# Optimization experiments

Measured on AMD Instinct MI355X. Metric: run time of the kernel, lower is better.

## Reference

```python
import jax, jax.numpy as jnp
import numpy as np

EPS = 1e-8
NMS_K = 15          # soft_nms_3d window
COM_NMS = 7.0       # soft_nms_3d com_strength
COM_SCORE = 100.0   # score_com_strength
COM_SCALE = 100.0   # scale_com_strength


def conv2d(x, w, b=None, pad=1, groups=1):
    y = jax.lax.conv_general_dilated(
        x, w, (1, 1), [(pad, pad), (pad, pad)],
        dimension_numbers=('NCHW', 'OIHW', 'NCHW'),
        feature_group_count=groups)
    if b is not None:
        y = y + b[None, :, None, None]
    return y


def bn(x, s, b):  # folded inference batchnorm: scale + shift per channel
    return x * s[None, :, None, None] + b[None, :, None, None]


def maxpool_same(x, k):
    p = k // 2
    return jax.lax.reduce_window(x, -jnp.inf, jax.lax.max,
                                 (1, 1, k, k), (1, 1, 1, 1),
                                 [(0, 0), (0, 0), (p, p), (p, p)])


def boxsum_same(x, k):
    p = k // 2
    return jax.lax.reduce_window(x, 0.0, jax.lax.add,
                                 (1, 1, k, k), (1, 1, 1, 1),
                                 [(0, 0), (0, 0), (p, p), (p, p)])


def instance_norm(x, eps=1e-5):  # no affine (nn.InstanceNorm2d default)
    mu = x.mean(axis=(2, 3), keepdims=True)
    var = x.var(axis=(2, 3), keepdims=True)
    return (x - mu) * jax.lax.rsqrt(var + eps)


def inverted_residual(x, dw_w, bna_s, bna_b, pw_w, bnb_s, bnb_b):
    # expand_ratio=1, stride=1, inp==oup -> residual connection
    h = conv2d(x, dw_w, pad=1, groups=x.shape[1])
    h = jnp.clip(bn(h, bna_s, bna_b), 0.0, 6.0)       # ReLU6
    h = conv2d(h, pw_w, pad=0)
    h = bn(h, bnb_s, bnb_b)
    return x + h


def forward(photos, w0, b0, dw1_w, bn1a_s, bn1a_b, pw1_w, bn1b_s, bn1b_b,
            dw2_w, bn2a_s, bn2a_b, pw2_w, bn2b_s, bn2b_b, ws, bs, scale_list):
    x = conv2d(photos, w0, b0)                                   # (B,16,H,W)
    x = inverted_residual(x, dw1_w, bn1a_s, bn1a_b, pw1_w, bn1b_s, bn1b_b)
    x = inverted_residual(x, dw2_w, bn2a_s, bn2a_b, pw2_w, bn2b_s, bn2b_b)
    s = conv2d(x, ws, bs)                                        # (B,C,H,W) C=scales
    s = jax.nn.leaky_relu(instance_norm(s), negative_slope=0.01)

    # ---- soft_nms_3d: windowed competitive softmax over (scale, 15x15) ----
    m = maxpool_same(s, NMS_K).max(axis=1, keepdims=True)        # (B,1,H,W)
    e = jnp.exp(COM_NMS * (s - m))                               # (B,C,H,W)
    sum_e = boxsum_same(e.sum(axis=1, keepdims=True), NMS_K)     # (B,1,H,W)
    probs = e / (sum_e + EPS)                                    # (B,C,H,W)

    # ---- soft_max_and_argmax_1d over scale dim ----
    mx = probs.max(axis=1, keepdims=True)
    e1 = jnp.exp(COM_SCORE * (probs - mx))
    p1 = e1 / (e1.sum(axis=1, keepdims=True) + EPS)
    e2 = jnp.exp(COM_SCALE * (probs - mx))
    p2 = e2 / (e2.sum(axis=1, keepdims=True) + EPS)
    score_map = (probs * p1).sum(axis=1, keepdims=True)          # (B,1,H,W)
    scale_map = (scale_list[None, :, None, None] * p2).sum(axis=1, keepdims=True)
    # return channel-last like the torch code (B,H,W,1)
    return (score_map.transpose(0, 2, 3, 1), scale_map.transpose(0, 2, 3, 1))


def setup_inputs() -> dict:
    key = jax.random.key(0)
    ks = jax.random.split(key, 20)
    B, H, W, C, S = 4, 512, 512, 16, 10
    rn = lambda k, sh, sc=0.1: (jax.random.normal(k, sh, jnp.float32) * sc)
    inp = {
        'photos': jax.random.normal(ks[0], (B, 1, H, W), jnp.float32),
        'w0': rn(ks[1], (C, 1, 3, 3)), 'b0': rn(ks[2], (C,)),
        'dw1_w': rn(ks[3], (C, 1, 3, 3)),
        'bn1a_s': jax.random.uniform(ks[4], (C,), jnp.float32, 0.5, 1.5),
        'bn1a_b': rn(ks[5], (C,)),
        'pw1_w': rn(ks[6], (C, C, 1, 1)),
        'bn1b_s': jax.random.uniform(ks[7], (C,), jnp.float32, 0.5, 1.5),
        'bn1b_b': rn(ks[8], (C,)),
        'dw2_w': rn(ks[9], (C, 1, 3, 3)),
        'bn2a_s': jax.random.uniform(ks[10], (C,), jnp.float32, 0.5, 1.5),
        'bn2a_b': rn(ks[11], (C,)),
        'pw2_w': rn(ks[12], (C, C, 1, 1)),
        'bn2b_s': jax.random.uniform(ks[13], (C,), jnp.float32, 0.5, 1.5),
        'bn2b_b': rn(ks[14], (C,)),
        'ws': rn(ks[15], (S, C, 3, 3)), 'bs': rn(ks[16], (S,)),
        'scale_list': jnp.linspace(3.0, 21.0, S, dtype=jnp.float32),
    }
    return inp


def reference(photos, w0, b0, dw1_w, bn1a_s, bn1a_b, pw1_w, bn1b_s, bn1b_b,
              dw2_w, bn2a_s, bn2a_b, pw2_w, bn2b_s, bn2b_b, ws, bs, scale_list):
    return forward(photos, w0, b0, dw1_w, bn1a_s, bn1a_b, pw1_w, bn1b_s, bn1b_b,
                   dw2_w, bn2a_s, bn2a_b, pw2_w, bn2b_s, bn2b_b, ws, bs, scale_list)
```

## Files before the change

### kernel.cpp

```cpp
#include <hip/hip_runtime.h>
#include <hip/hip_bf16.h>

#define Bn 4
#define Hn 512
#define Wn 512
#define Cn 16
#define Sn 10
#define HWn (Hn*Wn)
#define BHW (Bn*HWn)
#define NG (BHW/4)

__device__ __forceinline__ void load_row6(const float* __restrict__ rp, bool valid,
                                          int w0, float* r) {
    if (valid) {
        float4 v = *reinterpret_cast<const float4*>(rp + w0);
        r[1] = v.x; r[2] = v.y; r[3] = v.z; r[4] = v.w;
        r[0] = (w0 > 0)   ? rp[w0 - 1] : 0.f;
        r[5] = (w0 < 508) ? rp[w0 + 4] : 0.f;
    } else {
        r[0] = r[1] = r[2] = r[3] = r[4] = r[5] = 0.f;
    }
}

__global__ __launch_bounds__(256) void k_conv0(const float* __restrict__ photos,
        const float* __restrict__ w0v, const float* __restrict__ b0,
        float* __restrict__ out) {
    __shared__ float wp[Cn*12];
    __shared__ float sb[Cn];
    int t = threadIdx.x;
    if (t < Cn*9) { int o = t / 9, k = t % 9; wp[o*12 + k] = w0v[t]; }
    if (t < Cn) sb[t] = b0[t];
    __syncthreads();
    int idx = blockIdx.x * 256 + t;
    int w0 = (idx & 127) << 2, h = (idx >> 7) & 511, b = idx >> 16;
    const float* pb = photos + (b << 18);
    float xr[3][6];
    #pragma unroll
    for (int dy = 0; dy < 3; ++dy) {
        int hh = h + dy - 1;
        load_row6(pb + (hh << 9), (unsigned)hh < 512u, w0, xr[dy]);
    }
    #pragma unroll
    for (int o = 0; o < Cn; ++o) {
        float4 wa = *(const float4*)&wp[o*12];
        float4 wb = *(const float4*)&wp[o*12 + 4];
        float wk8 = wp[o*12 + 8];
        float wk[9] = {wa.x, wa.y, wa.z, wa.w, wb.x, wb.y, wb.z, wb.w, wk8};
        float bv = sb[o];
        float a0 = bv, a1 = bv, a2 = bv, a3 = bv;
        #pragma unroll
        for (int dy = 0; dy < 3; ++dy)
            #pragma unroll
            for (int dx = 0; dx < 3; ++dx) {
                float wv = wk[dy*3 + dx];
                a0 += xr[dy][dx + 0] * wv;
                a1 += xr[dy][dx + 1] * wv;
                a2 += xr[dy][dx + 2] * wv;
                a3 += xr[dy][dx + 3] * wv;
            }
        float4 r; r.x = a0; r.y = a1; r.z = a2; r.w = a3;
        *reinterpret_cast<float4*>(out + ((b*Cn + o) << 18) + (h << 9) + w0) = r;
    }
}


struct StageRegs { float4 b0, b1; float hl, hr; };

__device__ __forceinline__ StageRegs stage_load(const float* __restrict__ xc,
                                                int w0, int h0, int t) {
    StageRegs r;
    {
        int row = t >> 5, c4 = t & 31;
        int gh = h0 - 1 + row;
        r.b0 = make_float4(0.f, 0.f, 0.f, 0.f);
        if ((unsigned)gh < 512u)
            r.b0 = *reinterpret_cast<const float4*>(xc + (gh << 9) + w0 + (c4 << 2));
    }
    r.b1 = make_float4(0.f, 0.f, 0.f, 0.f);
    if (t < 64) {
        int s = t + 256;
        int row = s >> 5, c4 = s & 31;
        int gh = h0 - 1 + row;
        if ((unsigned)gh < 512u)
            r.b1 = *reinterpret_cast<const float4*>(xc + (gh << 9) + w0 + (c4 << 2));
    }
    r.hl = 0.f; r.hr = 0.f;
    if (t < 10) {
        int gh = h0 - 1 + t;
        if (w0 > 0 && (unsigned)gh < 512u) r.hl = xc[(gh << 9) + w0 - 1];
    }
    if (t >= 32 && t < 42) {
        int gh = h0 - 1 + (t - 32);
        if (w0 + 128 < 512 && (unsigned)gh < 512u) r.hr = xc[(gh << 9) + w0 + 128];
    }
    return r;
}

__device__ __forceinline__ void stage_write(float (*tile)[128], float* hL, float* hR,
                                            const StageRegs& r, int t) {
    *reinterpret_cast<float4*>(&tile[t >> 5][(t & 31) << 2]) = r.b0;
    if (t < 64) {
        int s = t + 256;
        *reinterpret_cast<float4*>(&tile[s >> 5][(s & 31) << 2]) = r.b1;
    }
    if (t < 10) hL[t] = r.hl;
    if (t >= 32 && t < 42) hR[t - 32] = r.hr;
}

#define READ_ROWS(tilebuf, hLbuf, hRbuf)                                        \
    float4 v_[3]; float lft_[3], rgt_[3];                                       \
    _Pragma("unroll")                                                           \
    for (int dy = 0; dy < 3; ++dy) {                                            \
        v_[dy] = *reinterpret_cast<const float4*>(&(tilebuf)[th + dy][tw << 2]);\
        float l_ = __shfl_up(v_[dy].w, 1);                                      \
        if (tw == 0) l_ = (hLbuf)[th + dy];                                     \
        float rr_ = __shfl_down(v_[dy].x, 1);                                   \
        if (tw == 31) rr_ = (hRbuf)[th + dy];                                   \
        lft_[dy] = l_; rgt_[dy] = rr_;                                          \
    }

__global__ __launch_bounds__(256) void k_ir(const float* __restrict__ x,
        float* __restrict__ y, const float* __restrict__ dww,
        const float* __restrict__ as_, const float* __restrict__ ab_,
        const float* __restrict__ pww, const float* __restrict__ bs_,
        const float* __restrict__ bb_) {
    __shared__ float tile[2][10][128];
    __shared__ float hLs[2][10], hRs[2][10];
    __shared__ float dwp[Cn*12];
    __shared__ float pwT[Cn*Cn];
    __shared__ float sas[Cn], sab[Cn], sbs[Cn], sbb[Cn];
    int t = threadIdx.x;
    { int o = t >> 4, i = t & 15; pwT[i*16 + o] = pww[t]; }
    if (t < Cn*9)  { int c = t / 9, k = t % 9; dwp[c*12 + k] = dww[t]; }
    if (t < Cn) { sas[t] = as_[t]; sab[t] = ab_[t]; }
    if (t >= 64 && t < 64 + Cn) { sbs[t-64] = bs_[t-64]; sbb[t-64] = bb_[t-64]; }

    int bx = blockIdx.x;
    int wt = bx & 3, ht = (bx >> 2) & 63, b = bx >> 8;
    int w0 = wt << 7, h0 = ht << 3;
    int tw = t & 31, th = t >> 5;
    const float* xb = x + ((size_t)b << 22);

    float acc[Cn][4];
    #pragma unroll
    for (int o = 0; o < Cn; ++o) { acc[o][0] = acc[o][1] = acc[o][2] = acc[o][3] = 0.f; }

    StageRegs sr = stage_load(xb, w0, h0, t);
    stage_write(tile[0], hLs[0], hRs[0], sr, t);
    __syncthreads();

    #pragma unroll 1
    for (int c = 0; c < Cn; ++c) {
        if (c + 1 < Cn) sr = stage_load(xb + ((c + 1) << 18), w0, h0, t);
        int bf = c & 1;
        READ_ROWS(tile[bf], hLs[bf], hRs[bf]);
        float4 wa = *(const float4*)&dwp[c*12];
        float4 wb = *(const float4*)&dwp[c*12 + 4];
        float wk8 = dwp[c*12 + 8];
        float wk[9] = {wa.x, wa.y, wa.z, wa.w, wb.x, wb.y, wb.z, wb.w, wk8};
        float t0 = 0.f, t1 = 0.f, t2 = 0.f, t3 = 0.f;
        #pragma unroll
        for (int dy = 0; dy < 3; ++dy) {
            float r6[6] = {lft_[dy], v_[dy].x, v_[dy].y, v_[dy].z, v_[dy].w, rgt_[dy]};
            #pragma unroll
            for (int dx = 0; dx < 3; ++dx) {
                float wv = wk[dy*3 + dx];
                t0 += r6[dx + 0] * wv;
                t1 += r6[dx + 1] * wv;
                t2 += r6[dx + 2] * wv;
                t3 += r6[dx + 3] * wv;
            }
        }
        float sc = sas[c], sh = sab[c];
        t0 = fminf(fmaxf(t0*sc + sh, 0.f), 6.f);
        t1 = fminf(fmaxf(t1*sc + sh, 0.f), 6.f);
        t2 = fminf(fmaxf(t2*sc + sh, 0.f), 6.f);
        t3 = fminf(fmaxf(t3*sc + sh, 0.f), 6.f);
        #pragma unroll
        for (int o4 = 0; o4 < 4; ++o4) {
            float4 wq = *(const float4*)&pwT[c*16 + o4*4];
            acc[o4*4+0][0] += t0*wq.x; acc[o4*4+0][1] += t1*wq.x;
            acc[o4*4+0][2] += t2*wq.x; acc[o4*4+0][3] += t3*wq.x;
            acc[o4*4+1][0] += t0*wq.y; acc[o4*4+1][1] += t1*wq.y;
            acc[o4*4+1][2] += t2*wq.y; acc[o4*4+1][3] += t3*wq.y;
            acc[o4*4+2][0] += t0*wq.z; acc[o4*4+2][1] += t1*wq.z;
            acc[o4*4+2][2] += t2*wq.z; acc[o4*4+2][3] += t3*wq.z;
            acc[o4*4+3][0] += t0*wq.w; acc[o4*4+3][1] += t1*wq.w;
            acc[o4*4+3][2] += t2*wq.w; acc[o4*4+3][3] += t3*wq.w;
        }
        if (c + 1 < Cn) {
            int nb = (c + 1) & 1;
            stage_write(tile[nb], hLs[nb], hRs[nb], sr, t);
            __syncthreads();
        }
    }
    int h = h0 + th, wg = w0 + (tw << 2);
    #pragma unroll
    for (int o = 0; o < Cn; ++o) {
        const float* xo = xb + (o << 18) + (h << 9) + wg;
        float4 xv = *(const float4*)xo;
        float sc = sbs[o], sh = sbb[o];
        float4 r;
        r.x = xv.x + acc[o][0]*sc + sh;
        r.y = xv.y + acc[o][1]*sc + sh;
        r.z = xv.z + acc[o][2]*sc + sh;
        r.w = xv.w + acc[o][3]*sc + sh;
        *reinterpret_cast<float4*>(y + ((size_t)b << 22) + (o << 18) + (h << 9) + wg) = r;
    }
}

__global__ __launch_bounds__(256) void k_convs(const float* __restrict__ x,
        const float* __restrict__ wsw, const float* __restrict__ bsv,
        float* __restrict__ s) {
    __shared__ float tile[2][10][128];
    __shared__ float hLs[2][10], hRs[2][10];
    __shared__ float wp[Cn*Sn*12];
    __shared__ float sb[Sn];
    int t = threadIdx.x;
    for (int i = t; i < Sn*Cn*9; i += 256) {
        int o = i / (Cn*9), r = i % (Cn*9), c = r / 9, k = r % 9;
        wp[(c*Sn + o)*12 + k] = wsw[i];
    }
    if (t < Sn) sb[t] = bsv[t];

    int bx = blockIdx.x;
    int wt = bx & 3, ht = (bx >> 2) & 63, b = bx >> 8;
    int w0 = wt << 7, h0 = ht << 3;
    int tw = t & 31, th = t >> 5;
    const float* xb = x + ((size_t)b << 22);

    float acc[Sn][4];
    #pragma unroll
    for (int o = 0; o < Sn; ++o) {
        float bv = bsv[o];
        acc[o][0] = bv; acc[o][1] = bv; acc[o][2] = bv; acc[o][3] = bv;
    }

    StageRegs sr = stage_load(xb, w0, h0, t);
    stage_write(tile[0], hLs[0], hRs[0], sr, t);
    __syncthreads();

    #pragma unroll 1
    for (int c = 0; c < Cn; ++c) {
        if (c + 1 < Cn) sr = stage_load(xb + ((c + 1) << 18), w0, h0, t);
        int bf = c & 1;
        READ_ROWS(tile[bf], hLs[bf], hRs[bf]);
        #pragma unroll
        for (int o = 0; o < Sn; ++o) {
            const float* wb_ = &wp[(c*Sn + o)*12];
            float4 wa = *(const float4*)wb_;
            float4 wv2 = *(const float4*)(wb_ + 4);
            float wk8 = wb_[8];
            float wk[9] = {wa.x, wa.y, wa.z, wa.w, wv2.x, wv2.y, wv2.z, wv2.w, wk8};
            #pragma unroll
            for (int dy = 0; dy < 3; ++dy) {
                float r6[6] = {lft_[dy], v_[dy].x, v_[dy].y, v_[dy].z, v_[dy].w, rgt_[dy]};
                #pragma unroll
                for (int dx = 0; dx < 3; ++dx) {
                    float wv = wk[dy*3 + dx];
                    acc[o][0] += r6[dx + 0] * wv;
                    acc[o][1] += r6[dx + 1] * wv;
                    acc[o][2] += r6[dx + 2] * wv;
                    acc[o][3] += r6[dx + 3] * wv;
                }
            }
        }
        if (c + 1 < Cn) {
            int nb = (c + 1) & 1;
            stage_write(tile[nb], hLs[nb], hRs[nb], sr, t);
            __syncthreads();
        }
    }
    int h = h0 + th, wg = w0 + (tw << 2);
    #pragma unroll
    for (int o = 0; o < Sn; ++o) {
        float4 r; r.x = acc[o][0]; r.y = acc[o][1]; r.z = acc[o][2]; r.w = acc[o][3];
        *reinterpret_cast<float4*>(s + ((b*Sn + o) << 18) + (h << 9) + wg) = r;
    }
}

__global__ __launch_bounds__(256) void k_in_part(const float* __restrict__ s,
                                                 double* __restrict__ part) {
    int bc = blockIdx.x >> 5, ch = blockIdx.x & 31;
    const float4* p4 = (const float4*)(s + ((size_t)bc << 18) + (ch << 13));
    int t = threadIdx.x;
    double sum = 0.0, sq = 0.0;
    #pragma unroll
    for (int i = 0; i < 8; ++i) {
        float4 v = p4[t + i * 256];
        sum += (double)v.x + (double)v.y + (double)v.z + (double)v.w;
        sq  += (double)v.x*v.x + (double)v.y*v.y + (double)v.z*v.z + (double)v.w*v.w;
    }
    __shared__ double ssum[256], ssq[256];
    ssum[t] = sum; ssq[t] = sq;
    __syncthreads();
    for (int off = 128; off > 0; off >>= 1) {
        if (t < off) { ssum[t] += ssum[t + off]; ssq[t] += ssq[t + off]; }
        __syncthreads();
    }
    if (t == 0) {
        part[blockIdx.x * 2]     = ssum[0];
        part[blockIdx.x * 2 + 1] = ssq[0];
    }
}

__global__ __launch_bounds__(64) void k_in_fin(const double* __restrict__ part,
                                               float2* __restrict__ stats) {
    int bc = blockIdx.x;
    int t = threadIdx.x;
    double sum = 0.0, sq = 0.0;
    if (t < 32) { sum = part[(bc * 32 + t) * 2]; sq = part[(bc * 32 + t) * 2 + 1]; }
    #pragma unroll
    for (int off = 32; off > 0; off >>= 1) {
        sum += __shfl_xor(sum, off);
        sq  += __shfl_xor(sq, off);
    }
    if (t == 0) {
        double mu = sum / (double)HWn;
        double var = sq / (double)HWn - mu * mu;
        float2 st; st.x = (float)mu; st.y = rsqrtf((float)var + 1e-5f);
        stats[bc] = st;
    }
}

__device__ __forceinline__ float nrm(float v, float2 st) {
    float r = (v - st.x) * st.y;
    return r >= 0.f ? r : 0.01f * r;
}

__global__ __launch_bounds__(256) void k_chan_rowmax(const float* __restrict__ s,
        const float2* __restrict__ stats, float* __restrict__ m1) {
    __shared__ float rowbuf[512];
    int bh = blockIdx.x;
    int b = bh >> 9, h = bh & 511;
    int t = threadIdx.x, w0 = t << 1;
    const float* sp = s + ((size_t)(b * Sn) << 18) + (h << 9) + w0;
    float mx0 = -INFINITY, mx1 = -INFINITY;
    #pragma unroll
    for (int c = 0; c < Sn; ++c) {
        float2 st = stats[b * Sn + c];
        float2 v = *reinterpret_cast<const float2*>(sp + ((size_t)c << 18));
        mx0 = fmaxf(mx0, nrm(v.x, st));
        mx1 = fmaxf(mx1, nrm(v.y, st));
    }
    rowbuf[w0] = mx0; rowbuf[w0 + 1] = mx1;
    __syncthreads();
    float2 o;
    {
        int lo = max(w0 - 7, 0), hi = min(w0 + 7, 511);
        float m = -INFINITY;
        for (int ww = lo; ww <= hi; ++ww) m = fmaxf(m, rowbuf[ww]);
        o.x = m;
        int w1 = w0 + 1;
        lo = max(w1 - 7, 0); hi = min(w1 + 7, 511);
        m = -INFINITY;
        for (int ww = lo; ww <= hi; ++ww) m = fmaxf(m, rowbuf[ww]);
        o.y = m;
    }
    *reinterpret_cast<float2*>(m1 + (bh << 9) + w0) = o;
}

__global__ __launch_bounds__(256) void k_col_expsum(const float* __restrict__ s,
        const float2* __restrict__ stats, const float* __restrict__ m1,
        float* __restrict__ mfull, float* __restrict__ tout) {
    __shared__ float esbuf[512];
    int bh = blockIdx.x;
    int b = bh >> 9, h = bh & 511;
    int t = threadIdx.x, w0 = t << 1;
    int lo = max(h - 7, 0), hi = min(h + 7, 511);
    float2 m = make_float2(-INFINITY, -INFINITY);
    for (int hh = lo; hh <= hi; ++hh) {
        float2 v = *reinterpret_cast<const float2*>(m1 + ((size_t)b << 18) + (hh << 9) + w0);
// ... 62 lines not shown
    #pragma unroll
    for (int c = 0; c < Sn; ++c) {
        e0[c] = expf(100.f * (pr0[c] - mx0)); s0 += e0[c];
        e1[c] = expf(100.f * (pr1[c] - mx1)); s1 += e1[c];
    }
    float i0 = 1.f / (s0 + 1e-8f), i1 = 1.f / (s1 + 1e-8f);
    float sc0 = 0.f, sc1 = 0.f, sl0 = 0.f, sl1 = 0.f;
    #pragma unroll
    for (int c = 0; c < Sn; ++c) {
        float p0 = e0[c] * i0, p1 = e1[c] * i1;
        sc0 += pr0[c] * p0; sl0 += sscale[c] * p0;
        sc1 += pr1[c] * p1; sl1 += sscale[c] * p1;
    }
    int oi = (bh << 9) + w0;
    float2 r0; r0.x = sc0; r0.y = sc1;
    float2 r1; r1.x = sl0; r1.y = sl1;
    *reinterpret_cast<float2*>(out + oi) = r0;
    *reinterpret_cast<float2*>(out + BHW + oi) = r1;
}

extern "C" void kernel_launch(void* const* d_in, const int* in_sizes, int n_in,
                              void* d_out, int out_size, void* d_ws, size_t ws_size,
                              hipStream_t stream) {
    const float* photos = (const float*)d_in[0];
    const float* w0     = (const float*)d_in[1];
    const float* b0     = (const float*)d_in[2];
    const float* dw1_w  = (const float*)d_in[3];
    const float* bn1a_s = (const float*)d_in[4];
    const float* bn1a_b = (const float*)d_in[5];
    const float* pw1_w  = (const float*)d_in[6];
    const float* bn1b_s = (const float*)d_in[7];
    const float* bn1b_b = (const float*)d_in[8];
    const float* dw2_w  = (const float*)d_in[9];
    const float* bn2a_s = (const float*)d_in[10];
    const float* bn2a_b = (const float*)d_in[11];
    const float* pw2_w  = (const float*)d_in[12];
    const float* bn2b_s = (const float*)d_in[13];
    const float* bn2b_b = (const float*)d_in[14];
    const float* ws_w   = (const float*)d_in[15];
    const float* bs_v   = (const float*)d_in[16];
    const float* scl    = (const float*)d_in[17];

    char* wsb = (char*)d_ws;
    float* A  = (float*)(wsb);
    float* Bb = (float*)(wsb + 67108864);
    float* S  = (float*)(wsb + 134217728);
    float2* stats = (float2*)Bb;
    double* part  = (double*)(Bb + 1024);
    float* M1 = A;
    float* M  = A + 1 * (1 << 20);
    float* T  = A + 2 * (1 << 20);

    dim3 blk(256);
    int gNG   = NG / 256;
    int gTILE = 4 * 64 * Bn;
    int gROW  = Bn * Hn;

    k_conv0<<<gNG, blk, 0, stream>>>(photos, w0, b0, A);
    k_ir<<<gTILE, blk, 0, stream>>>(A, Bb, dw1_w, bn1a_s, bn1a_b, pw1_w, bn1b_s, bn1b_b);
    k_ir<<<gTILE, blk, 0, stream>>>(Bb, A, dw2_w, bn2a_s, bn2a_b, pw2_w, bn2b_s, bn2b_b);
    k_convs<<<gTILE, blk, 0, stream>>>(A, ws_w, bs_v, S);
    k_in_part<<<Bn * Sn * 32, blk, 0, stream>>>(S, part);
    k_in_fin<<<Bn * Sn, dim3(64), 0, stream>>>(part, stats);
    k_chan_rowmax<<<gROW, blk, 0, stream>>>(S, stats, M1);
    k_col_expsum<<<gROW, blk, 0, stream>>>(S, stats, M1, M, T);
    k_final<<<gROW, blk, 0, stream>>>(S, stats, M, T, scl, (float*)d_out);
}
```

Measured before the change: 215.4 us.

## Retile IR and score convs to 4x128 tiles staging four channels per barrier

Changes the k_ir and k_convs tiling from 8x128 output tiles with 4 pixels per thread to 4x128 tiles with 2 pixels per thread, doubling the grid. Each pipeline stage now stages four input channels at once into padded shared rows with halo columns, replacing per-channel syncs and warp shuffles with direct shared-memory neighbour reads. The aim is fewer barriers, lower register pressure and higher occupancy. The cost is a larger vertical halo overhead (6 rows loaded per 4 output rows instead of 10 per 8) and narrower global stores.

```diff
diff --git a/kernel.cpp b/kernel.cpp
--- a/kernel.cpp
+++ b/kernel.cpp
@@ -64,59 +64,65 @@
 }
 
 
-struct StageRegs { float4 b0, b1; float hl, hr; };
-
-__device__ __forceinline__ StageRegs stage_load(const float* __restrict__ xc,
-                                                int w0, int h0, int t) {
-    StageRegs r;
+#define RSTR 132
+
+struct SR { float4 q0, q1, q2; float hl, hr; };
+
+__device__ __forceinline__ float4 body_ld(const float* __restrict__ base,
+                                          int s, int w0, int h0) {
+    int ch = s / 192, rem = s - ch * 192, rr = rem >> 5, q = rem & 31;
+    int gh = h0 - 1 + rr;
+    float4 v = make_float4(0.f, 0.f, 0.f, 0.f);
+    if ((unsigned)gh < 512u)
+        v = *reinterpret_cast<const float4*>(base + (ch << 18) + (gh << 9) + w0 + (q << 2));
+    return v;
+}
+
+__device__ __forceinline__ SR st_load(const float* __restrict__ base,
+                                      int w0, int h0, int t) {
+    SR r;
+    r.q0 = body_ld(base, t,       w0, h0);
+    r.q1 = body_ld(base, t + 256, w0, h0);
+    r.q2 = body_ld(base, t + 512, w0, h0);
+    r.hl = 0.f; r.hr = 0.f;
+    if (t < 24) {
+        int ch = t / 6, rr = t % 6, gh = h0 - 1 + rr;
+        if (w0 > 0 && (unsigned)gh < 512u) r.hl = base[(ch << 18) + (gh << 9) + w0 - 1];
+    }
+    if (t >= 64 && t < 88) {
+        int u = t - 64, ch = u / 6, rr = u % 6, gh = h0 - 1 + rr;
+        if (w0 + 128 < 512 && (unsigned)gh < 512u) r.hr = base[(ch << 18) + (gh << 9) + w0 + 128];
+    }
+    return r;
+}
+
+__device__ __forceinline__ void st_write(float* __restrict__ buf,
+                                         const SR& r, int t) {
     {
-        int row = t >> 5, c4 = t & 31;
-        int gh = h0 - 1 + row;
-        r.b0 = make_float4(0.f, 0.f, 0.f, 0.f);
-        if ((unsigned)gh < 512u)
-            r.b0 = *reinterpret_cast<const float4*>(xc + (gh << 9) + w0 + (c4 << 2));
-    }
-    r.b1 = make_float4(0.f, 0.f, 0.f, 0.f);
-    if (t < 64) {
-        int s = t + 256;
-        int row = s >> 5, c4 = s & 31;
-        int gh = h0 - 1 + row;
-        if ((unsigned)gh < 512u)
-            r.b1 = *reinterpret_cast<const float4*>(xc + (gh << 9) + w0 + (c4 << 2));
-    }
-    r.hl = 0.f; r.hr = 0.f;
-    if (t < 10) {
-        int gh = h0 - 1 + t;
-        if (w0 > 0 && (unsigned)gh < 512u) r.hl = xc[(gh << 9) + w0 - 1];
-    }
-    if (t >= 32 && t < 42) {
-        int gh = h0 - 1 + (t - 32);
-        if (w0 + 128 < 512 && (unsigned)gh < 512u) r.hr = xc[(gh << 9) + w0 + 128];
-    }
-    return r;
-}
-
-__device__ __forceinline__ void stage_write(float (*tile)[128], float* hL, float* hR,
-                                            const StageRegs& r, int t) {
-    *reinterpret_cast<float4*>(&tile[t >> 5][(t & 31) << 2]) = r.b0;
-    if (t < 64) {
-        int s = t + 256;
-        *reinterpret_cast<float4*>(&tile[s >> 5][(s & 31) << 2]) = r.b1;
-    }
-    if (t < 10) hL[t] = r.hl;
-    if (t >= 32 && t < 42) hR[t - 32] = r.hr;
-}
-
-#define READ_ROWS(tilebuf, hLbuf, hRbuf)                                        \
-    float4 v_[3]; float lft_[3], rgt_[3];                                       \
+        int s = t;       int ch = s / 192, rem = s - ch * 192, rr = rem >> 5, q = rem & 31;
+        *reinterpret_cast<float4*>(buf + (ch * 6 + rr) * RSTR + (q << 2)) = r.q0;
+    }
+    {
+        int s = t + 256; int ch = s / 192, rem = s - ch * 192, rr = rem >> 5, q = rem & 31;
+        *reinterpret_cast<float4*>(buf + (ch * 6 + rr) * RSTR + (q << 2)) = r.q1;
+    }
+    {
+        int s = t + 512; int ch = s / 192, rem = s - ch * 192, rr = rem >> 5, q = rem & 31;
+        *reinterpret_cast<float4*>(buf + (ch * 6 + rr) * RSTR + (q << 2)) = r.q2;
+    }
+    if (t < 24)              buf[((t / 6) * 6 + (t % 6)) * RSTR + 129] = r.hl;
+    if (t >= 64 && t < 88) { int u = t - 64; buf[((u / 6) * 6 + (u % 6)) * RSTR + 128] = r.hr; }
+}
+
+#define LOAD_X(bufp, j)                                                         \
+    float xl_[3], x0_[3], x1_[3], xr_[3];                                       \
     _Pragma("unroll")                                                           \
     for (int dy = 0; dy < 3; ++dy) {                                            \
-        v_[dy] = *reinterpret_cast<const float4*>(&(tilebuf)[th + dy][tw << 2]);\
-        float l_ = __shfl_up(v_[dy].w, 1);                                      \
-        if (tw == 0) l_ = (hLbuf)[th + dy];                                     \
-        float rr_ = __shfl_down(v_[dy].x, 1);                                   \
-        if (tw == 31) rr_ = (hRbuf)[th + dy];                                   \
-        lft_[dy] = l_; rgt_[dy] = rr_;                                          \
+        const float* rp_ = (bufp) + ((j) * 6 + row + dy) * RSTR;                \
+        float2 v_ = *reinterpret_cast<const float2*>(rp_ + 2 * col2);           \
+        x0_[dy] = v_.x; x1_[dy] = v_.y;                                         \
+        xr_[dy] = rp_[2 * col2 + 2];                                            \
+        xl_[dy] = (col2 == 0) ? rp_[129] : rp_[2 * col2 - 1];                   \
     }
 
 __global__ __launch_bounds__(256) void k_ir(const float* __restrict__ x,
@@ -124,8 +130,7 @@
         const float* __restrict__ as_, const float* __restrict__ ab_,
         const float* __restrict__ pww, const float* __restrict__ bs_,
         const float* __restrict__ bb_) {
-    __shared__ float tile[2][10][128];
-    __shared__ float hLs[2][10], hRs[2][10];
+    __shared__ float tile[2][4 * 6 * RSTR];
     __shared__ float dwp[Cn*12];
     __shared__ float pwT[Cn*Cn];
     __shared__ float sas[Cn], sab[Cn], sbs[Cn], sbb[Cn];
@@ -136,146 +141,133 @@
     if (t >= 64 && t < 64 + Cn) { sbs[t-64] = bs_[t-64]; sbb[t-64] = bb_[t-64]; }
 
     int bx = blockIdx.x;
-    int wt = bx & 3, ht = (bx >> 2) & 63, b = bx >> 8;
-    int w0 = wt << 7, h0 = ht << 3;
-    int tw = t & 31, th = t >> 5;
+    int wt = bx & 3, ht = (bx >> 2) & 127, b = bx >> 9;
+    int w0 = wt << 7, h0 = ht << 2;
+    int row = t >> 6, col2 = t & 63;
     const float* xb = x + ((size_t)b << 22);
 
-    float acc[Cn][4];
-    #pragma unroll
-    for (int o = 0; o < Cn; ++o) { acc[o][0] = acc[o][1] = acc[o][2] = acc[o][3] = 0.f; }
-
-    StageRegs sr = stage_load(xb, w0, h0, t);
-    stage_write(tile[0], hLs[0], hRs[0], sr, t);
+    float acc[Cn][2];
+    #pragma unroll
+    for (int o = 0; o < Cn; ++o) { acc[o][0] = 0.f; acc[o][1] = 0.f; }
+
+    SR sr = st_load(xb, w0, h0, t);
+    st_write(tile[0], sr, t);
     __syncthreads();
 
     #pragma unroll 1
-    for (int c = 0; c < Cn; ++c) {
-        if (c + 1 < Cn) sr = stage_load(xb + ((c + 1) << 18), w0, h0, t);
-        int bf = c & 1;
-        READ_ROWS(tile[bf], hLs[bf], hRs[bf]);
-        float4 wa = *(const float4*)&dwp[c*12];
-        float4 wb = *(const float4*)&dwp[c*12 + 4];
-        float wk8 = dwp[c*12 + 8];
-        float wk[9] = {wa.x, wa.y, wa.z, wa.w, wb.x, wb.y, wb.z, wb.w, wk8};
-        float t0 = 0.f, t1 = 0.f, t2 = 0.f, t3 = 0.f;
+    for (int g = 0; g < 4; ++g) {
+        SR nxt;
+        bool more = (g + 1 < 4);
+        if (more) nxt = st_load(xb + ((g + 1) * 4 << 18), w0, h0, t);
+        const float* bufp = tile[g & 1];
         #pragma unroll
-        for (int dy = 0; dy < 3; ++dy) {
-            float r6[6] = {lft_[dy], v_[dy].x, v_[dy].y, v_[dy].z, v_[dy].w, rgt_[dy]};
+        for (int j = 0; j < 4; ++j) {
+            int cc = g * 4 + j;
+            LOAD_X(bufp, j);
+            float4 wa = *(const float4*)&dwp[cc*12];
+            float4 wb = *(const float4*)&dwp[cc*12 + 4];
+            float wk8 = dwp[cc*12 + 8];
+            float wk[9] = {wa.x, wa.y, wa.z, wa.w, wb.x, wb.y, wb.z, wb.w, wk8};
+            float t0 = 0.f, t1 = 0.f;
             #pragma unroll
-            for (int dx = 0; dx < 3; ++dx) {
-                float wv = wk[dy*3 + dx];
-                t0 += r6[dx + 0] * wv;
-                t1 += r6[dx + 1] * wv;
-                t2 += r6[dx + 2] * wv;
-                t3 += r6[dx + 3] * wv;
+            for (int dy = 0; dy < 3; ++dy) {
+                float k0 = wk[dy*3], k1 = wk[dy*3+1], k2 = wk[dy*3+2];
+                t0 += xl_[dy]*k0 + x0_[dy]*k1 + x1_[dy]*k2;
+                t1 += x0_[dy]*k0 + x1_[dy]*k1 + xr_[dy]*k2;
+            }
+            float sc = sas[cc], sh = sab[cc];
+            t0 = fminf(fmaxf(t0*sc + sh, 0.f), 6.f);
+            t1 = fminf(fmaxf(t1*sc + sh, 0.f), 6.f);
+            #pragma unroll
+            for (int o4 = 0; o4 < 4; ++o4) {
+                float4 wq = *(const float4*)&pwT[cc*16 + o4*4];
+                acc[o4*4+0][0] += t0*wq.x; acc[o4*4+0][1] += t1*wq.x;
+                acc[o4*4+1][0] += t0*wq.y; acc[o4*4+1][1] += t1*wq.y;
+                acc[o4*4+2][0] += t0*wq.z; acc[o4*4+2][1] += t1*wq.z;
+                acc[o4*4+3][0] += t0*wq.w; acc[o4*4+3][1] += t1*wq.w;
             }
         }
-        float sc = sas[c], sh = sab[c];
-        t0 = fminf(fmaxf(t0*sc + sh, 0.f), 6.f);
-        t1 = fminf(fmaxf(t1*sc + sh, 0.f), 6.f);
-        t2 = fminf(fmaxf(t2*sc + sh, 0.f), 6.f);
-        t3 = fminf(fmaxf(t3*sc + sh, 0.f), 6.f);
-        #pragma unroll
-        for (int o4 = 0; o4 < 4; ++o4) {
-            float4 wq = *(const float4*)&pwT[c*16 + o4*4];
-            acc[o4*4+0][0] += t0*wq.x; acc[o4*4+0][1] += t1*wq.x;
-            acc[o4*4+0][2] += t2*wq.x; acc[o4*4+0][3] += t3*wq.x;
-            acc[o4*4+1][0] += t0*wq.y; acc[o4*4+1][1] += t1*wq.y;
-            acc[o4*4+1][2] += t2*wq.y; acc[o4*4+1][3] += t3*wq.y;
-            acc[o4*4+2][0] += t0*wq.z; acc[o4*4+2][1] += t1*wq.z;
-            acc[o4*4+2][2] += t2*wq.z; acc[o4*4+2][3] += t3*wq.z;
-            acc[o4*4+3][0] += t0*wq.w; acc[o4*4+3][1] += t1*wq.w;
-            acc[o4*4+3][2] += t2*wq.w; acc[o4*4+3][3] += t3*wq.w;
-        }
-        if (c + 1 < Cn) {
-            int nb = (c + 1) & 1;
-            stage_write(tile[nb], hLs[nb], hRs[nb], sr, t);
+        if (more) {
+            st_write(tile[(g + 1) & 1], nxt, t);
             __syncthreads();
         }
     }
-    int h = h0 + th, wg = w0 + (tw << 2);
+    int h = h0 + row, wg = w0 + (col2 << 1);
     #pragma unroll
     for (int o = 0; o < Cn; ++o) {
-        const float* xo = xb + (o << 18) + (h << 9) + wg;
-        float4 xv = *(const float4*)xo;
+        size_t oi = ((size_t)b << 22) + (o << 18) + (h << 9) + wg;
+        float2 xv = *reinterpret_cast<const float2*>(x + oi);
         float sc = sbs[o], sh = sbb[o];
-        float4 r;
+        float2 r;
         r.x = xv.x + acc[o][0]*sc + sh;
         r.y = xv.y + acc[o][1]*sc + sh;
-        r.z = xv.z + acc[o][2]*sc + sh;
-        r.w = xv.w + acc[o][3]*sc + sh;
-        *reinterpret_cast<float4*>(y + ((size_t)b << 22) + (o << 18) + (h << 9) + wg) = r;
+        *reinterpret_cast<float2*>(y + oi) = r;
     }
 }
 
 __global__ __launch_bounds__(256) void k_convs(const float* __restrict__ x,
         const float* __restrict__ wsw, const float* __restrict__ bsv,
         float* __restrict__ s) {
-    __shared__ float tile[2][10][128];
-    __shared__ float hLs[2][10], hRs[2][10];
+    __shared__ float tile[2][4 * 6 * RSTR];
     __shared__ float wp[Cn*Sn*12];
-    __shared__ float sb[Sn];
     int t = threadIdx.x;
     for (int i = t; i < Sn*Cn*9; i += 256) {
         int o = i / (Cn*9), r = i % (Cn*9), c = r / 9, k = r % 9;
         wp[(c*Sn + o)*12 + k] = wsw[i];
     }
-    if (t < Sn) sb[t] = bsv[t];
 
     int bx = blockIdx.x;
-    int wt = bx & 3, ht = (bx >> 2) & 63, b = bx >> 8;
-    int w0 = wt << 7, h0 = ht << 3;
-    int tw = t & 31, th = t >> 5;
+    int wt = bx & 3, ht = (bx >> 2) & 127, b = bx >> 9;
+    int w0 = wt << 7, h0 = ht << 2;
+    int row = t >> 6, col2 = t & 63;
     const float* xb = x + ((size_t)b << 22);
 
-    float acc[Sn][4];
+    float acc[Sn][2];
     #pragma unroll
     for (int o = 0; o < Sn; ++o) {
         float bv = bsv[o];
-        acc[o][0] = bv; acc[o][1] = bv; acc[o][2] = bv; acc[o][3] = bv;
-    }
-
-    StageRegs sr = stage_load(xb, w0, h0, t);
-    stage_write(tile[0], hLs[0], hRs[0], sr, t);
+        acc[o][0] = bv; acc[o][1] = bv;
+    }
+
+    SR sr = st_load(xb, w0, h0, t);
+    st_write(tile[0], sr, t);
     __syncthreads();
 
     #pragma unroll 1
-    for (int c = 0; c < Cn; ++c) {
-        if (c + 1 < Cn) sr = stage_load(xb + ((c + 1) << 18), w0, h0, t);
-        int bf = c & 1;
-        READ_ROWS(tile[bf], hLs[bf], hRs[bf]);
+    for (int g = 0; g < 4; ++g) {
+        SR nxt;
+        bool more = (g + 1 < 4);
+        if (more) nxt = st_load(xb + ((g + 1) * 4 << 18), w0, h0, t);
+        const float* bufp = tile[g & 1];
         #pragma unroll
-        for (int o = 0; o < Sn; ++o) {
-            const float* wb_ = &wp[(c*Sn + o)*12];
-            float4 wa = *(const float4*)wb_;
-            float4 wv2 = *(const float4*)(wb_ + 4);
-            float wk8 = wb_[8];
-            float wk[9] = {wa.x, wa.y, wa.z, wa.w, wv2.x, wv2.y, wv2.z, wv2.w, wk8};
+        for (int j = 0; j < 4; ++j) {
+            int cc = g * 4 + j;
+            LOAD_X(bufp, j);
             #pragma unroll
-            for (int dy = 0; dy < 3; ++dy) {
-                float r6[6] = {lft_[dy], v_[dy].x, v_[dy].y, v_[dy].z, v_[dy].w, rgt_[dy]};
+            for (int o = 0; o < Sn; ++o) {
+                const float* wb_ = &wp[(cc*Sn + o)*12];
+                float4 wa = *(const float4*)wb_;
+                float4 wv2 = *(const float4*)(wb_ + 4);
+                float wk8 = wb_[8];
+                float wk[9] = {wa.x, wa.y, wa.z, wa.w, wv2.x, wv2.y, wv2.z, wv2.w, wk8};
                 #pragma unroll
-                for (int dx = 0; dx < 3; ++dx) {
-                    float wv = wk[dy*3 + dx];
-                    acc[o][0] += r6[dx + 0] * wv;
-                    acc[o][1] += r6[dx + 1] * wv;
-                    acc[o][2] += r6[dx + 2] * wv;
-                    acc[o][3] += r6[dx + 3] * wv;
+                for (int dy = 0; dy < 3; ++dy) {
+                    float k0 = wk[dy*3], k1 = wk[dy*3+1], k2 = wk[dy*3+2];
+                    acc[o][0] += xl_[dy]*k0 + x0_[dy]*k1 + x1_[dy]*k2;
+                    acc[o][1] += x0_[dy]*k0 + x1_[dy]*k1 + xr_[dy]*k2;
                 }
             }
         }
-        if (c + 1 < Cn) {
-            int nb = (c + 1) & 1;
-            stage_write(tile[nb], hLs[nb], hRs[nb], sr, t);
+        if (more) {
+            st_write(tile[(g + 1) & 1], nxt, t);
             __syncthreads();
         }
     }
-    int h = h0 + th, wg = w0 + (tw << 2);
+    int h = h0 + row, wg = w0 + (col2 << 1);
     #pragma unroll
     for (int o = 0; o < Sn; ++o) {
-        float4 r; r.x = acc[o][0]; r.y = acc[o][1]; r.z = acc[o][2]; r.w = acc[o][3];
-        *reinterpret_cast<float4*>(s + ((b*Sn + o) << 18) + (h << 9) + wg) = r;
+        float2 r; r.x = acc[o][0]; r.y = acc[o][1];
+        *reinterpret_cast<float2*>(s + ((size_t)(b*Sn + o) << 18) + (h << 9) + wg) = r;
     }
 }
 
@@ -487,7 +479,7 @@
 
     dim3 blk(256);
     int gNG   = NG / 256;
-    int gTILE = 4 * 64 * Bn;
+    int gTILE = 4 * 128 * Bn;
     int gROW  = Bn * Hn;
 
     k_conv0<<<gNG, blk, 0, stream>>>(photos, w0, b0, A);
```

After: 428.8 us. 99.1% more time.

## Fuse first conv into first inverted residual and fold residual into accumulator

Applied to the files above, without the earlier changes.

The initial 3x3 conv is now recomputed per tile inside the first inverted-residual kernel from a photo patch in shared memory, so the 16-channel intermediate is never written to or read back from global memory. The residual add is folded into the pointwise accumulator by pre-adding x scaled by the reciprocal of the BN scale, which removes the extra global read of x at the end of each IR kernel. The cost is redundant conv0 arithmetic on halo pixels, higher register use from the 5x8 patch, and a division by the BN scale that can misbehave if a scale is near zero.

```diff
diff --git a/kernel.cpp b/kernel.cpp
--- a/kernel.cpp
+++ b/kernel.cpp
@@ -8,58 +8,152 @@
 #define Sn 10
 #define HWn (Hn*Wn)
 #define BHW (Bn*HWn)
-#define NG (BHW/4)
-
-__device__ __forceinline__ void load_row6(const float* __restrict__ rp, bool valid,
-                                          int w0, float* r) {
-    if (valid) {
-        float4 v = *reinterpret_cast<const float4*>(rp + w0);
-        r[1] = v.x; r[2] = v.y; r[3] = v.z; r[4] = v.w;
-        r[0] = (w0 > 0)   ? rp[w0 - 1] : 0.f;
-        r[5] = (w0 < 508) ? rp[w0 + 4] : 0.f;
-    } else {
-        r[0] = r[1] = r[2] = r[3] = r[4] = r[5] = 0.f;
-    }
-}
-
-__global__ __launch_bounds__(256) void k_conv0(const float* __restrict__ photos,
+
+__global__ __launch_bounds__(256) void k_c0ir1(const float* __restrict__ photos,
         const float* __restrict__ w0v, const float* __restrict__ b0,
-        float* __restrict__ out) {
-    __shared__ float wp[Cn*12];
-    __shared__ float sb[Cn];
+        const float* __restrict__ dww, const float* __restrict__ as_,
+        const float* __restrict__ ab_, const float* __restrict__ pww,
+        const float* __restrict__ bs_, const float* __restrict__ bb_,
+        float* __restrict__ y) {
+    __shared__ float P[12][132];
+    __shared__ float c0w[Cn*12];
+    __shared__ float c0b[Cn];
+    __shared__ float dwp[Cn*12];
+    __shared__ float pwT[Cn*Cn];
+    __shared__ float sas[Cn], sab[Cn], sbs[Cn], sbb[Cn], sbi[Cn];
     int t = threadIdx.x;
-    if (t < Cn*9) { int o = t / 9, k = t % 9; wp[o*12 + k] = w0v[t]; }
-    if (t < Cn) sb[t] = b0[t];
+    { int o = t >> 4, i = t & 15; pwT[i*16 + o] = pww[t]; }
+    if (t < Cn*9) {
+        int c = t / 9, k = t % 9;
+        c0w[c*12 + k] = w0v[t];
+        dwp[c*12 + k] = dww[t];
+    }
+    if (t < Cn) {
+        c0b[t] = b0[t]; sas[t] = as_[t]; sab[t] = ab_[t];
+        float s2 = bs_[t];
+        sbs[t] = s2; sbb[t] = bb_[t]; sbi[t] = 1.f / s2;
+    }
+
+    int bx = blockIdx.x;
+    int wt = bx & 3, ht = (bx >> 2) & 63, b = bx >> 8;
+    int w0 = wt << 7, h0 = ht << 3;
+    int tw = t & 31, th = t >> 5;
+    const float* pb = photos + ((size_t)b << 18);
+
+    {
+        int s = t;
+        {
+            int row = s >> 5, q = s & 31, gh = h0 - 2 + row;
+            float4 v = make_float4(0.f, 0.f, 0.f, 0.f);
+            if ((unsigned)gh < 512u)
+                v = *reinterpret_cast<const float4*>(pb + (gh << 9) + w0 + (q << 2));
+            *reinterpret_cast<float4*>(&P[row][q << 2]) = v;
+        }
+        if (t < 128) {
+            int s2 = t + 256;
+            int row = s2 >> 5, q = s2 & 31, gh = h0 - 2 + row;
+            float4 v = make_float4(0.f, 0.f, 0.f, 0.f);
+            if ((unsigned)gh < 512u)
+                v = *reinterpret_cast<const float4*>(pb + (gh << 9) + w0 + (q << 2));
+            *reinterpret_cast<float4*>(&P[row][q << 2]) = v;
+        }
+        if (t < 48) {
+            int cid = t / 12, row = t % 12;
+            const int cdel[4]  = {-2, -1, 128, 129};
+            const int lidx[4]  = {130, 131, 128, 129};
+            int c = cdel[cid], gh = h0 - 2 + row, gc = w0 + c;
+            float v = 0.f;
+            if ((unsigned)gh < 512u && (unsigned)gc < 512u) v = pb[(gh << 9) + gc];
+            P[row][lidx[cid]] = v;
+        }
+    }
     __syncthreads();
-    int idx = blockIdx.x * 256 + t;
-    int w0 = (idx & 127) << 2, h = (idx >> 7) & 511, b = idx >> 16;
-    const float* pb = photos + (b << 18);
-    float xr[3][6];
-    #pragma unroll
-    for (int dy = 0; dy < 3; ++dy) {
-        int hh = h + dy - 1;
-        load_row6(pb + (hh << 9), (unsigned)hh < 512u, w0, xr[dy]);
+
+    int h = h0 + th;
+    int wg = w0 + (tw << 2);
+    float patch[5][8];
+    #pragma unroll
+    for (int j = 0; j < 5; ++j) {
+        #pragma unroll
+        for (int i = 0; i < 8; ++i) {
+            int c = (tw << 2) - 2 + i;
+            int idx = (c >= 0) ? c : (132 + c);
+            patch[j][i] = P[th + j][idx];
+        }
+    }
+
+    float acc[Cn][4];
+    #pragma unroll
+    for (int o = 0; o < Cn; ++o) { acc[o][0] = acc[o][1] = acc[o][2] = acc[o][3] = 0.f; }
+
+    #pragma unroll 1
+    for (int cc = 0; cc < Cn; ++cc) {
+        float4 ca = *(const float4*)&c0w[cc*12];
+        float4 cb4 = *(const float4*)&c0w[cc*12 + 4];
+        float cw8 = c0w[cc*12 + 8];
+        float cw[9] = {ca.x, ca.y, ca.z, ca.w, cb4.x, cb4.y, cb4.z, cb4.w, cw8};
+        float cbv = c0b[cc];
+        float cv[3][6];
+        #pragma unroll
+        for (int ry = 0; ry < 3; ++ry) {
+            bool rok = (unsigned)(h - 1 + ry) < 512u;
+            #pragma unroll
+            for (int cx = 0; cx < 6; ++cx) {
+                bool cok = (unsigned)(wg - 1 + cx) < 512u;
+                float a = cbv;
+                #pragma unroll
+                for (int j = 0; j < 3; ++j)
+                    #pragma unroll
+                    for (int i = 0; i < 3; ++i)
+                        a += patch[ry + j][cx + i] * cw[j*3 + i];
+                cv[ry][cx] = (rok && cok) ? a : 0.f;
+            }
+        }
+        float4 wa = *(const float4*)&dwp[cc*12];
+        float4 wb = *(const float4*)&dwp[cc*12 + 4];
+        float wk8 = dwp[cc*12 + 8];
+        float wk[9] = {wa.x, wa.y, wa.z, wa.w, wb.x, wb.y, wb.z, wb.w, wk8};
+        float t0 = 0.f, t1 = 0.f, t2 = 0.f, t3 = 0.f;
+        #pragma unroll
+        for (int ry = 0; ry < 3; ++ry) {
+            float k0 = wk[ry*3], k1 = wk[ry*3+1], k2 = wk[ry*3+2];
+            t0 += cv[ry][0]*k0 + cv[ry][1]*k1 + cv[ry][2]*k2;
+            t1 += cv[ry][1]*k0 + cv[ry][2]*k1 + cv[ry][3]*k2;
+            t2 += cv[ry][2]*k0 + cv[ry][3]*k1 + cv[ry][4]*k2;
+            t3 += cv[ry][3]*k0 + cv[ry][4]*k1 + cv[ry][5]*k2;
+        }
+        float sc = sas[cc], sh = sab[cc];
+        t0 = fminf(fmaxf(t0*sc + sh, 0.f), 6.f);
+        t1 = fminf(fmaxf(t1*sc + sh, 0.f), 6.f);
+        t2 = fminf(fmaxf(t2*sc + sh, 0.f), 6.f);
+        t3 = fminf(fmaxf(t3*sc + sh, 0.f), 6.f);
+        float ri = sbi[cc];
+        acc[cc][0] += cv[1][1] * ri;
+        acc[cc][1] += cv[1][2] * ri;
+        acc[cc][2] += cv[1][3] * ri;
+        acc[cc][3] += cv[1][4] * ri;
+        #pragma unroll
+        for (int o4 = 0; o4 < 4; ++o4) {
+            float4 wq = *(const float4*)&pwT[cc*16 + o4*4];
+            acc[o4*4+0][0] += t0*wq.x; acc[o4*4+0][1] += t1*wq.x;
+            acc[o4*4+0][2] += t2*wq.x; acc[o4*4+0][3] += t3*wq.x;
+            acc[o4*4+1][0] += t0*wq.y; acc[o4*4+1][1] += t1*wq.y;
+            acc[o4*4+1][2] += t2*wq.y; acc[o4*4+1][3] += t3*wq.y;
+            acc[o4*4+2][0] += t0*wq.z; acc[o4*4+2][1] += t1*wq.z;
+            acc[o4*4+2][2] += t2*wq.z; acc[o4*4+2][3] += t3*wq.z;
+            acc[o4*4+3][0] += t0*wq.w; acc[o4*4+3][1] += t1*wq.w;
+            acc[o4*4+3][2] += t2*wq.w; acc[o4*4+3][3] += t3*wq.w;
+        }
     }
     #pragma unroll
     for (int o = 0; o < Cn; ++o) {
-        float4 wa = *(const float4*)&wp[o*12];
-        float4 wb = *(const float4*)&wp[o*12 + 4];
-        float wk8 = wp[o*12 + 8];
-        float wk[9] = {wa.x, wa.y, wa.z, wa.w, wb.x, wb.y, wb.z, wb.w, wk8};
-        float bv = sb[o];
-        float a0 = bv, a1 = bv, a2 = bv, a3 = bv;
-        #pragma unroll
-        for (int dy = 0; dy < 3; ++dy)
-            #pragma unroll
-            for (int dx = 0; dx < 3; ++dx) {
-                float wv = wk[dy*3 + dx];
-                a0 += xr[dy][dx + 0] * wv;
-                a1 += xr[dy][dx + 1] * wv;
-                a2 += xr[dy][dx + 2] * wv;
-                a3 += xr[dy][dx + 3] * wv;
-            }
-        float4 r; r.x = a0; r.y = a1; r.z = a2; r.w = a3;
-        *reinterpret_cast<float4*>(out + ((b*Cn + o) << 18) + (h << 9) + w0) = r;
+        float sc = sbs[o], sh = sbb[o];
+        float4 r;
+        r.x = acc[o][0]*sc + sh;
+        r.y = acc[o][1]*sc + sh;
+        r.z = acc[o][2]*sc + sh;
+        r.w = acc[o][3]*sc + sh;
+        *reinterpret_cast<float4*>(y + ((size_t)(b*Cn + o) << 18) + (h << 9) + wg) = r;
     }
 }
 
@@ -128,12 +222,15 @@
     __shared__ float hLs[2][10], hRs[2][10];
     __shared__ float dwp[Cn*12];
     __shared__ float pwT[Cn*Cn];
-    __shared__ float sas[Cn], sab[Cn], sbs[Cn], sbb[Cn];
+    __shared__ float sas[Cn], sab[Cn], sbs[Cn], sbb[Cn], sbi[Cn];
     int t = threadIdx.x;
     { int o = t >> 4, i = t & 15; pwT[i*16 + o] = pww[t]; }
     if (t < Cn*9)  { int c = t / 9, k = t % 9; dwp[c*12 + k] = dww[t]; }
     if (t < Cn) { sas[t] = as_[t]; sab[t] = ab_[t]; }
-    if (t >= 64 && t < 64 + Cn) { sbs[t-64] = bs_[t-64]; sbb[t-64] = bb_[t-64]; }
+    if (t >= 64 && t < 64 + Cn) {
+        float s2 = bs_[t-64];
+        sbs[t-64] = s2; sbb[t-64] = bb_[t-64]; sbi[t-64] = 1.f / s2;
+    }
 
     int bx = blockIdx.x;
     int wt = bx & 3, ht = (bx >> 2) & 63, b = bx >> 8;
@@ -176,6 +273,11 @@
         t1 = fminf(fmaxf(t1*sc + sh, 0.f), 6.f);
         t2 = fminf(fmaxf(t2*sc + sh, 0.f), 6.f);
         t3 = fminf(fmaxf(t3*sc + sh, 0.f), 6.f);
+        float ri = sbi[c];
+        acc[c][0] += v_[1].x * ri;
+        acc[c][1] += v_[1].y * ri;
+        acc[c][2] += v_[1].z * ri;
+        acc[c][3] += v_[1].w * ri;
         #pragma unroll
         for (int o4 = 0; o4 < 4; ++o4) {
             float4 wq = *(const float4*)&pwT[c*16 + o4*4];
@@ -197,14 +299,12 @@
     int h = h0 + th, wg = w0 + (tw << 2);
     #pragma unroll
     for (int o = 0; o < Cn; ++o) {
-        const float* xo = xb + (o << 18) + (h << 9) + wg;
-        float4 xv = *(const float4*)xo;
         float sc = sbs[o], sh = sbb[o];
         float4 r;
-        r.x = xv.x + acc[o][0]*sc + sh;
-        r.y = xv.y + acc[o][1]*sc + sh;
-        r.z = xv.z + acc[o][2]*sc + sh;
-        r.w = xv.w + acc[o][3]*sc + sh;
+        r.x = acc[o][0]*sc + sh;
+        r.y = acc[o][1]*sc + sh;
+        r.z = acc[o][2]*sc + sh;
+        r.w = acc[o][3]*sc + sh;
         *reinterpret_cast<float4*>(y + ((size_t)b << 22) + (o << 18) + (h << 9) + wg) = r;
     }
 }
@@ -486,14 +586,13 @@
     float* T  = A + 2 * (1 << 20);
 
     dim3 blk(256);
-    int gNG   = NG / 256;
     int gTILE = 4 * 64 * Bn;
     int gROW  = Bn * Hn;
 
-    k_conv0<<<gNG, blk, 0, stream>>>(photos, w0, b0, A);
-    k_ir<<<gTILE, blk, 0, stream>>>(A, Bb, dw1_w, bn1a_s, bn1a_b, pw1_w, bn1b_s, bn1b_b);
-    k_ir<<<gTILE, blk, 0, stream>>>(Bb, A, dw2_w, bn2a_s, bn2a_b, pw2_w, bn2b_s, bn2b_b);
-    k_convs<<<gTILE, blk, 0, stream>>>(A, ws_w, bs_v, S);
+    k_c0ir1<<<gTILE, blk, 0, stream>>>(photos, w0, b0, dw1_w, bn1a_s, bn1a_b,
+                                       pw1_w, bn1b_s, bn1b_b, A);
+    k_ir<<<gTILE, blk, 0, stream>>>(A, Bb, dw2_w, bn2a_s, bn2a_b, pw2_w, bn2b_s, bn2b_b);
+    k_convs<<<gTILE, blk, 0, stream>>>(Bb, ws_w, bs_v, S);
     k_in_part<<<Bn * Sn * 32, blk, 0, stream>>>(S, part);
     k_in_fin<<<Bn * Sn, dim3(64), 0, stream>>>(part, stats);
     k_chan_rowmax<<<gROW, blk, 0, stream>>>(S, stats, M1);
```

Result: slower. 769.2 us (+257.2%).

## Fuse instance-norm partial sums into scale conv and reuse tile for residual

Applied to the files above, without the earlier changes.

The instance-norm sum and sum-of-squares are now computed inside the scale convolution kernel via wavefront shuffles, which removes the separate reduction pass that re-read the whole score tensor. The finish kernel now reduces 256 per-block partials per channel. In the inverted-residual kernel, the residual input is taken from the already-loaded tile center row and pre-divided by the BN scale, so the extra global read of x at the end is avoided. This relies on the BN scale being nonzero and slightly changes rounding.

```diff
diff --git a/kernel.cpp b/kernel.cpp
--- a/kernel.cpp
+++ b/kernel.cpp
@@ -128,12 +128,15 @@
     __shared__ float hLs[2][10], hRs[2][10];
     __shared__ float dwp[Cn*12];
     __shared__ float pwT[Cn*Cn];
-    __shared__ float sas[Cn], sab[Cn], sbs[Cn], sbb[Cn];
+    __shared__ float sas[Cn], sab[Cn], sbs[Cn], sbb[Cn], sbi[Cn];
     int t = threadIdx.x;
     { int o = t >> 4, i = t & 15; pwT[i*16 + o] = pww[t]; }
     if (t < Cn*9)  { int c = t / 9, k = t % 9; dwp[c*12 + k] = dww[t]; }
     if (t < Cn) { sas[t] = as_[t]; sab[t] = ab_[t]; }
-    if (t >= 64 && t < 64 + Cn) { sbs[t-64] = bs_[t-64]; sbb[t-64] = bb_[t-64]; }
+    if (t >= 64 && t < 64 + Cn) {
+        float s2 = bs_[t-64];
+        sbs[t-64] = s2; sbb[t-64] = bb_[t-64]; sbi[t-64] = 1.f / s2;
+    }
 
     int bx = blockIdx.x;
     int wt = bx & 3, ht = (bx >> 2) & 63, b = bx >> 8;
@@ -176,6 +179,11 @@
         t1 = fminf(fmaxf(t1*sc + sh, 0.f), 6.f);
         t2 = fminf(fmaxf(t2*sc + sh, 0.f), 6.f);
         t3 = fminf(fmaxf(t3*sc + sh, 0.f), 6.f);
+        float ri = sbi[c];
+        acc[c][0] += v_[1].x * ri;
+        acc[c][1] += v_[1].y * ri;
+        acc[c][2] += v_[1].z * ri;
+        acc[c][3] += v_[1].w * ri;
         #pragma unroll
         for (int o4 = 0; o4 < 4; ++o4) {
             float4 wq = *(const float4*)&pwT[c*16 + o4*4];
@@ -197,25 +205,24 @@
     int h = h0 + th, wg = w0 + (tw << 2);
     #pragma unroll
     for (int o = 0; o < Cn; ++o) {
-        const float* xo = xb + (o << 18) + (h << 9) + wg;
-        float4 xv = *(const float4*)xo;
         float sc = sbs[o], sh = sbb[o];
         float4 r;
-        r.x = xv.x + acc[o][0]*sc + sh;
-        r.y = xv.y + acc[o][1]*sc + sh;
-        r.z = xv.z + acc[o][2]*sc + sh;
-        r.w = xv.w + acc[o][3]*sc + sh;
+        r.x = acc[o][0]*sc + sh;
+        r.y = acc[o][1]*sc + sh;
+        r.z = acc[o][2]*sc + sh;
+        r.w = acc[o][3]*sc + sh;
         *reinterpret_cast<float4*>(y + ((size_t)b << 22) + (o << 18) + (h << 9) + wg) = r;
     }
 }
 
 __global__ __launch_bounds__(256) void k_convs(const float* __restrict__ x,
         const float* __restrict__ wsw, const float* __restrict__ bsv,
-        float* __restrict__ s) {
+        float* __restrict__ s, double* __restrict__ part) {
     __shared__ float tile[2][10][128];
     __shared__ float hLs[2][10], hRs[2][10];
     __shared__ float wp[Cn*Sn*12];
     __shared__ float sb[Sn];
+    __shared__ double wsum[4][Sn], wsq[4][Sn];
     int t = threadIdx.x;
     for (int i = t; i < Sn*Cn*9; i += 256) {
         int o = i / (Cn*9), r = i % (Cn*9), c = r / 9, k = r % 9;
@@ -277,47 +284,46 @@
         float4 r; r.x = acc[o][0]; r.y = acc[o][1]; r.z = acc[o][2]; r.w = acc[o][3];
         *reinterpret_cast<float4*>(s + ((b*Sn + o) << 18) + (h << 9) + wg) = r;
     }
-}
-
-__global__ __launch_bounds__(256) void k_in_part(const float* __restrict__ s,
-                                                 double* __restrict__ part) {
-    int bc = blockIdx.x >> 5, ch = blockIdx.x & 31;
-    const float4* p4 = (const float4*)(s + ((size_t)bc << 18) + (ch << 13));
-    int t = threadIdx.x;
-    double sum = 0.0, sq = 0.0;
-    #pragma unroll
-    for (int i = 0; i < 8; ++i) {
-        float4 v = p4[t + i * 256];
-        sum += (double)v.x + (double)v.y + (double)v.z + (double)v.w;
-        sq  += (double)v.x*v.x + (double)v.y*v.y + (double)v.z*v.z + (double)v.w*v.w;
-    }
-    __shared__ double ssum[256], ssq[256];
-    ssum[t] = sum; ssq[t] = sq;
-    __syncthreads();
-    for (int off = 128; off > 0; off >>= 1) {
-        if (t < off) { ssum[t] += ssum[t + off]; ssq[t] += ssq[t + off]; }
-        __syncthreads();
-    }
-    if (t == 0) {
-        part[blockIdx.x * 2]     = ssum[0];
-        part[blockIdx.x * 2 + 1] = ssq[0];
-    }
-}
-
-__global__ __launch_bounds__(64) void k_in_fin(const double* __restrict__ part,
-                                               float2* __restrict__ stats) {
+    int lane = t & 63, wid = t >> 6;
+    #pragma unroll
+    for (int o = 0; o < Sn; ++o) {
+        double sm = (double)acc[o][0] + (double)acc[o][1]
+                  + (double)acc[o][2] + (double)acc[o][3];
+        double qq = (double)acc[o][0]*acc[o][0] + (double)acc[o][1]*acc[o][1]
+                  + (double)acc[o][2]*acc[o][2] + (double)acc[o][3]*acc[o][3];
+        #pragma unroll
+        for (int off = 32; off > 0; off >>= 1) {
+            sm += __shfl_xor(sm, off);
+            qq += __shfl_xor(qq, off);
+        }
+        if (lane == 0) { wsum[wid][o] = sm; wsq[wid][o] = qq; }
+    }
+    __syncthreads();
+    if (t < Sn) {
+        double sm = wsum[0][t] + wsum[1][t] + wsum[2][t] + wsum[3][t];
+        double qq = wsq[0][t] + wsq[1][t] + wsq[2][t] + wsq[3][t];
+        int blk = bx & 255;
+        int idx = ((b * Sn + t) << 8) + blk;
+        part[idx * 2]     = sm;
+        part[idx * 2 + 1] = qq;
+    }
+}
+
+__global__ __launch_bounds__(256) void k_in_fin(const double* __restrict__ part,
+                                                float2* __restrict__ stats) {
+    __shared__ double ss[256], qq[256];
     int bc = blockIdx.x;
     int t = threadIdx.x;
-    double sum = 0.0, sq = 0.0;
-    if (t < 32) { sum = part[(bc * 32 + t) * 2]; sq = part[(bc * 32 + t) * 2 + 1]; }
-    #pragma unroll
-    for (int off = 32; off > 0; off >>= 1) {
-        sum += __shfl_xor(sum, off);
-        sq  += __shfl_xor(sq, off);
+    ss[t] = part[((bc << 8) + t) * 2];
+    qq[t] = part[((bc << 8) + t) * 2 + 1];
+    __syncthreads();
+    for (int off = 128; off > 0; off >>= 1) {
+        if (t < off) { ss[t] += ss[t + off]; qq[t] += qq[t + off]; }
+        __syncthreads();
     }
     if (t == 0) {
-        double mu = sum / (double)HWn;
-        double var = sq / (double)HWn - mu * mu;
+        double mu = ss[0] / (double)HWn;
+        double var = qq[0] / (double)HWn - mu * mu;
         float2 st; st.x = (float)mu; st.y = rsqrtf((float)var + 1e-5f);
         stats[bc] = st;
     }
@@ -493,9 +499,8 @@
     k_conv0<<<gNG, blk, 0, stream>>>(photos, w0, b0, A);
     k_ir<<<gTILE, blk, 0, stream>>>(A, Bb, dw1_w, bn1a_s, bn1a_b, pw1_w, bn1b_s, bn1b_b);
     k_ir<<<gTILE, blk, 0, stream>>>(Bb, A, dw2_w, bn2a_s, bn2a_b, pw2_w, bn2b_s, bn2b_b);
-    k_convs<<<gTILE, blk, 0, stream>>>(A, ws_w, bs_v, S);
-    k_in_part<<<Bn * Sn * 32, blk, 0, stream>>>(S, part);
-    k_in_fin<<<Bn * Sn, dim3(64), 0, stream>>>(part, stats);
+    k_convs<<<gTILE, blk, 0, stream>>>(A, ws_w, bs_v, S, part);
+    k_in_fin<<<Bn * Sn, blk, 0, stream>>>(part, stats);
     k_chan_rowmax<<<gROW, blk, 0, stream>>>(S, stats, M1);
     k_col_expsum<<<gROW, blk, 0, stream>>>(S, stats, M1, M, T);
     k_final<<<gROW, blk, 0, stream>>>(S, stats, M, T, scl, (float*)d_out);
```

Measured after the change: 687.1 us. 219% more time.
